# Kernel tuning notes

Hardware: AMD Instinct MI355X
Metric: run time of the kernel (lower is better)

## Reference

```python
import jax, jax.numpy as jnp
from jax import lax
import numpy as np

WIN = 9  # default window [9, 9] in the original module


def _box_sum(x, win):
    """Sum over a win x win window, stride 1, pad win//2 (same as conv2d with ones kernel).
    Implemented separably (two 1D convs) - mathematically identical to the 2D ones-kernel conv.
    x: [B, 1, H, W] float32.
    """
    pad = win // 2
    kh = jnp.ones((1, 1, win, 1), x.dtype)
    kw = jnp.ones((1, 1, 1, win), x.dtype)
    dn = lax.conv_dimension_numbers(x.shape, kh.shape, ('NCHW', 'OIHW', 'NCHW'))
    y = lax.conv_general_dilated(x, kh, (1, 1), [(pad, pad), (0, 0)], dimension_numbers=dn)
    return lax.conv_general_dilated(y, kw, (1, 1), [(0, 0), (pad, pad)], dimension_numbers=dn)


def setup_inputs() -> dict:
    key = jax.random.key(0)
    k1, k2 = jax.random.split(key)
    shape = (32, 1, 512, 512)
    predict = jax.random.uniform(k1, shape, dtype=jnp.float32)
    target = jax.random.uniform(k2, shape, dtype=jnp.float32)
    return {"predict": predict, "target": target}


def reference(predict, target):
    win = WIN
    win_size = jnp.asarray(win * win, jnp.float32)

    I, J = predict, target
    I_sum = _box_sum(I, win)
    J_sum = _box_sum(J, win)
    I2_sum = _box_sum(I * I, win)
    J2_sum = _box_sum(J * J, win)
    IJ_sum = _box_sum(I * J, win)

    u_I = I_sum / win_size
    u_J = J_sum / win_size

    cross = IJ_sum - u_J * I_sum - u_I * J_sum + u_I * u_J * win_size
    I_var = I2_sum - 2.0 * u_I * I_sum + u_I * u_I * win_size
    J_var = J2_sum - 2.0 * u_J * J_sum + u_J * u_J * win_size

    cc = cross * cross / (I_var * J_var + 1e-6)
    return -jnp.mean(cc) + 1.0
```

## Files before the change

### kernel.cpp

```cpp
#include <hip/hip_runtime.h>


#define W 512
#define H 512
#define BH 8
#define NBANDS (H / BH)
#define NT 64

__device__ __forceinline__ float4 ld4(const float* p) {
    return *reinterpret_cast<const float4*>(p);
}

#define DECLBUF(P) float4 P##A0, P##A1, P##B0, P##B1; float P##m

#define LOADR(P, DR) do {                                                    \
    int _r  = y0 + (DR);                                                     \
    int _rc = _r < 0 ? 0 : (_r > (H - 1) ? (H - 1) : _r);                    \
    const float* _ip = Ip + _rc * W + x0;                                    \
    const float* _jp = Jp + _rc * W + x0;                                    \
    P##A0 = ld4(_ip);  P##A1 = ld4(_ip + 4);                                 \
    P##B0 = ld4(_jp);  P##B1 = ld4(_jp + 4);                                 \
    P##m  = (_r == _rc) ? 1.f : 0.f;                                         \
} while (0)

#define PBODY(P, OP)                                                         \
    do {                                                                     \
        float _m = P##m;                                                     \
        float _a0=P##A0.x*_m, _a1=P##A0.y*_m, _a2=P##A0.z*_m, _a3=P##A0.w*_m;\
        float _a4=P##A1.x*_m, _a5=P##A1.y*_m, _a6=P##A1.z*_m, _a7=P##A1.w*_m;\
        float _b0=P##B0.x*_m, _b1=P##B0.y*_m, _b2=P##B0.z*_m, _b3=P##B0.w*_m;\
        float _b4=P##B1.x*_m, _b5=P##B1.y*_m, _b6=P##B1.z*_m, _b7=P##B1.w*_m;\
        v0[0] OP _a0; v0[1] OP _a1; v0[2] OP _a2; v0[3] OP _a3;              \
        v0[4] OP _a4; v0[5] OP _a5; v0[6] OP _a6; v0[7] OP _a7;              \
        v1[0] OP _b0; v1[1] OP _b1; v1[2] OP _b2; v1[3] OP _b3;              \
        v1[4] OP _b4; v1[5] OP _b5; v1[6] OP _b6; v1[7] OP _b7;              \
        v2[0] OP _a0*P##A0.x; v2[1] OP _a1*P##A0.y; v2[2] OP _a2*P##A0.z; v2[3] OP _a3*P##A0.w; \
        v2[4] OP _a4*P##A1.x; v2[5] OP _a5*P##A1.y; v2[6] OP _a6*P##A1.z; v2[7] OP _a7*P##A1.w; \
        v3[0] OP _b0*P##B0.x; v3[1] OP _b1*P##B0.y; v3[2] OP _b2*P##B0.z; v3[3] OP _b3*P##B0.w; \
        v3[4] OP _b4*P##B1.x; v3[5] OP _b5*P##B1.y; v3[6] OP _b6*P##B1.z; v3[7] OP _b7*P##B1.w; \
        v4[0] OP _a0*P##B0.x; v4[1] OP _a1*P##B0.y; v4[2] OP _a2*P##B0.z; v4[3] OP _a3*P##B0.w; \
        v4[4] OP _a4*P##B1.x; v4[5] OP _a5*P##B1.y; v4[6] OP _a6*P##B1.z; v4[7] OP _a7*P##B1.w; \
    } while (0)

#define PADD(P) PBODY(P, +=)
#define PSUB(P) PBODY(P, -=)

#define HLO(vv, h, l7out) do {                                               \
    float _l4 = __shfl_up(vv[4], 1), _l5 = __shfl_up(vv[5], 1);              \
    float _l6 = __shfl_up(vv[6], 1), _l7 = __shfl_up(vv[7], 1);              \
    if (lane == 0) { _l4 = 0.f; _l5 = 0.f; _l6 = 0.f; _l7 = 0.f; }           \
    float _t = (((_l4+_l5)+(_l6+_l7)) + ((vv[0]+vv[1])+(vv[2]+vv[3]))) + vv[4]; \
    h[0] = _t;                                                               \
    _t += vv[5] - _l4; h[1] = _t;                                            \
    _t += vv[6] - _l5; h[2] = _t;                                            \
    _t += vv[7] - _l6; h[3] = _t;                                            \
    l7out = _l7;                                                             \
} while (0)

#define HHI(vv, h3in, l7in, h) do {                                          \
    float _r0 = __shfl_down(vv[0], 1), _r1 = __shfl_down(vv[1], 1);          \
    float _r2 = __shfl_down(vv[2], 1), _r3 = __shfl_down(vv[3], 1);          \
    if (lane == 63) { _r0 = 0.f; _r1 = 0.f; _r2 = 0.f; _r3 = 0.f; }          \
    float _t = (h3in) + _r0 - (l7in); h[0] = _t;                             \
    _t += _r1 - vv[0]; h[1] = _t;                                            \
    _t += _r2 - vv[1]; h[2] = _t;                                            \
    _t += _r3 - vv[2]; h[3] = _t;                                            \
} while (0)

#define CC4(h0a, h1a, h2a, h3a, h4a) do {                                    \
    _Pragma("unroll")                                                        \
    for (int _c = 0; _c < 4; ++_c) {                                         \
        float _Is = h0a[_c], _Js = h1a[_c];                                  \
        float _u  = _Is * inv81;                                             \
        float _cr = h4a[_c] - _u * _Js;                                      \
        float _Iv = h2a[_c] - _u * _Is;                                      \
        float _Jv = h3a[_c] - (_Js * inv81) * _Js;                           \
        cc_acc += (_cr * _cr) * __builtin_amdgcn_rcpf(_Iv * _Jv + 1e-6f);    \
    }                                                                        \
} while (0)

#define EPI() do {                                                           \
    float h0[4], h1[4], h2[4], h3[4], h4[4];                                 \
    float s0, s1, s2, s3, s4;                                                \
    HLO(v0, h0, s0); HLO(v1, h1, s1); HLO(v2, h2, s2);                       \
    HLO(v3, h3, s3); HLO(v4, h4, s4);                                        \
    CC4(h0, h1, h2, h3, h4);                                                 \
    float e0 = h0[3], e1 = h1[3], e2 = h2[3], e3 = h3[3], e4 = h4[3];        \
    HHI(v0, e0, s0, h0); HHI(v1, e1, s1, h1); HHI(v2, e2, s2, h2);           \
    HHI(v3, e3, s3, h3); HHI(v4, e4, s4, h4);                                \
    CC4(h0, h1, h2, h3, h4);                                                 \
} while (0)

#define STEPL(AB, SB, DR) do { PADD(AB); EPI(); PSUB(SB); LOADR(SB, DR); } while (0)
#define STEPN(AB, SB)     do { PADD(AB); EPI(); PSUB(SB); } while (0)

__global__ __launch_bounds__(NT, 2)
void ncc_main(const float* __restrict__ I, const float* __restrict__ J,
              float* __restrict__ partials) {
    const int lane = threadIdx.x & 63;

    const int nblk = gridDim.x;
    const int g = (blockIdx.x & 7) * (nblk >> 3) + (blockIdx.x >> 3);

    const int b    = g >> 6;
    const int band = g & (NBANDS - 1);
    const int y0   = band * BH;
    const float* Ip = I + (size_t)b * (H * W);
    const float* Jp = J + (size_t)b * (H * W);
    const int x0 = lane * 8;

    float v0[8], v1[8], v2[8], v3[8], v4[8];
    #pragma unroll
    for (int k = 0; k < 8; ++k) { v0[k]=0.f; v1[k]=0.f; v2[k]=0.f; v3[k]=0.f; v4[k]=0.f; }

    float cc_acc = 0.f;
    const float inv81 = 1.f / 81.f;

    DECLBUF(B0); DECLBUF(B1); DECLBUF(B2); DECLBUF(B3); DECLBUF(B4);
    DECLBUF(B5); DECLBUF(B6); DECLBUF(B7); DECLBUF(B8); DECLBUF(B9);

    LOADR(B0, -4); LOADR(B1, -3); LOADR(B2, -2); LOADR(B3, -1);
    LOADR(B4,  0); LOADR(B5,  1); LOADR(B6,  2); LOADR(B7,  3);
    LOADR(B8,  4); LOADR(B9,  5);

    PADD(B0); PADD(B1); PADD(B2); PADD(B3);
    PADD(B4); PADD(B5); PADD(B6); PADD(B7);

    STEPL(B8, B0,  6);
    STEPL(B9, B1,  7);
    STEPL(B0, B2,  8);
    STEPL(B1, B3,  9);
    STEPL(B2, B4, 10);
    STEPL(B3, B5, 11);
    STEPN(B4, B6);
    STEPN(B5, B7);

    #pragma unroll
    for (int off = 32; off > 0; off >>= 1)
        cc_acc += __shfl_down(cc_acc, off, 64);
    if (lane == 0) partials[blockIdx.x] = cc_acc;
}

__global__ __launch_bounds__(256)
void ncc_finish(const float* __restrict__ partials, float* __restrict__ out,
                int n, float inv_total) {
    float v = 0.f;
    for (int i = threadIdx.x; i < n; i += blockDim.x) v += partials[i];
    #pragma unroll
    for (int off = 32; off > 0; off >>= 1)
        v += __shfl_down(v, off, 64);
    __shared__ float wsum[4];
    if ((threadIdx.x & 63) == 0) wsum[threadIdx.x >> 6] = v;
    __syncthreads();
    if (threadIdx.x == 0) {
        float t = (wsum[0] + wsum[1]) + (wsum[2] + wsum[3]);
        out[0] = 1.0f - t * inv_total;
    }
}

extern "C" void kernel_launch(void* const* d_in, const int* in_sizes, int n_in,
                              void* d_out, int out_size, void* d_ws, size_t ws_size,
                              hipStream_t stream) {
    const float* I = (const float*)d_in[0];
    const float* J = (const float*)d_in[1];
    float* out = (float*)d_out;
    float* partials = (float*)d_ws;

    const int n = in_sizes[0];
    const int B = n / (H * W);
    const int nblocks = B * NBANDS;

    ncc_main<<<nblocks, NT, 0, stream>>>(I, J, partials);
    ncc_finish<<<1, 256, 0, stream>>>(partials, out, nblocks, 1.0f / (float)n);
}
```

Measured before the change: 108.1 us.

## Widen row bands to 32 rows with deeper 12-row register prefetch ring

Each single-wavefront block now processes a 32-row band instead of 8, cutting halo re-reads from 8 extra rows per 8 output rows to 8 per 32. The sliding-window ring grows from 10 to 12 row buffers so loads are issued four steps ahead, and the min-blocks launch bound is dropped. Grid size falls fourfold, to 512 one-wave blocks, which lowers occupancy and parallelism on a GPU with many CUs. Register pressure also rises.

```diff
diff --git a/kernel.cpp b/kernel.cpp
--- a/kernel.cpp
+++ b/kernel.cpp
@@ -3,7 +3,7 @@
 
 #define W 512
 #define H 512
-#define BH 8
+#define BH 32
 #define NBANDS (H / BH)
 #define NT 64
 
@@ -94,7 +94,7 @@
 #define STEPL(AB, SB, DR) do { PADD(AB); EPI(); PSUB(SB); LOADR(SB, DR); } while (0)
 #define STEPN(AB, SB)     do { PADD(AB); EPI(); PSUB(SB); } while (0)
 
-__global__ __launch_bounds__(NT, 2)
+__global__ __launch_bounds__(NT)
 void ncc_main(const float* __restrict__ I, const float* __restrict__ J,
               float* __restrict__ partials) {
     const int lane = threadIdx.x & 63;
@@ -102,7 +102,7 @@
     const int nblk = gridDim.x;
     const int g = (blockIdx.x & 7) * (nblk >> 3) + (blockIdx.x >> 3);
 
-    const int b    = g >> 6;
+    const int b    = g >> 4;
     const int band = g & (NBANDS - 1);
     const int y0   = band * BH;
     const float* Ip = I + (size_t)b * (H * W);
@@ -116,24 +116,49 @@
     float cc_acc = 0.f;
     const float inv81 = 1.f / 81.f;
 
-    DECLBUF(B0); DECLBUF(B1); DECLBUF(B2); DECLBUF(B3); DECLBUF(B4);
-    DECLBUF(B5); DECLBUF(B6); DECLBUF(B7); DECLBUF(B8); DECLBUF(B9);
-
-    LOADR(B0, -4); LOADR(B1, -3); LOADR(B2, -2); LOADR(B3, -1);
-    LOADR(B4,  0); LOADR(B5,  1); LOADR(B6,  2); LOADR(B7,  3);
-    LOADR(B8,  4); LOADR(B9,  5);
+    DECLBUF(B0); DECLBUF(B1); DECLBUF(B2);  DECLBUF(B3);
+    DECLBUF(B4); DECLBUF(B5); DECLBUF(B6);  DECLBUF(B7);
+    DECLBUF(B8); DECLBUF(B9); DECLBUF(B10); DECLBUF(B11);
+
+    LOADR(B0, -4); LOADR(B1, -3); LOADR(B2,   -2); LOADR(B3,  -1);
+    LOADR(B4,  0); LOADR(B5,  1); LOADR(B6,    2); LOADR(B7,   3);
+    LOADR(B8,  4); LOADR(B9,  5); LOADR(B10,   6); LOADR(B11,  7);
 
     PADD(B0); PADD(B1); PADD(B2); PADD(B3);
     PADD(B4); PADD(B5); PADD(B6); PADD(B7);
 
-    STEPL(B8, B0,  6);
-    STEPL(B9, B1,  7);
-    STEPL(B0, B2,  8);
-    STEPL(B1, B3,  9);
-    STEPL(B2, B4, 10);
-    STEPL(B3, B5, 11);
-    STEPN(B4, B6);
-    STEPN(B5, B7);
+    STEPL(B8,  B0,   8);
+    STEPL(B9,  B1,   9);
+    STEPL(B10, B2,  10);
+    STEPL(B11, B3,  11);
+    STEPL(B0,  B4,  12);
+    STEPL(B1,  B5,  13);
+    STEPL(B2,  B6,  14);
+    STEPL(B3,  B7,  15);
+    STEPL(B4,  B8,  16);
+    STEPL(B5,  B9,  17);
+    STEPL(B6,  B10, 18);
+    STEPL(B7,  B11, 19);
+    STEPL(B8,  B0,  20);
+    STEPL(B9,  B1,  21);
+    STEPL(B10, B2,  22);
+    STEPL(B11, B3,  23);
+    STEPL(B0,  B4,  24);
+    STEPL(B1,  B5,  25);
+    STEPL(B2,  B6,  26);
+    STEPL(B3,  B7,  27);
+    STEPL(B4,  B8,  28);
+    STEPL(B5,  B9,  29);
+    STEPL(B6,  B10, 30);
+    STEPL(B7,  B11, 31);
+    STEPL(B8,  B0,  32);
+    STEPL(B9,  B1,  33);
+    STEPL(B10, B2,  34);
+    STEPL(B11, B3,  35);
+    STEPN(B0,  B4);
+    STEPN(B1,  B5);
+    STEPN(B2,  B6);
+    STEPN(B3,  B7);
 
     #pragma unroll
     for (int off = 32; off > 0; off >>= 1)
```

After: 122.0 us. 1.13x slower.

## Double band height and stream rows through small register ring with reloads

Applied to the files above, without the earlier changes.

The band height per wavefront goes from 8 to 16 rows, which halves the number of blocks and cuts the halo overhead (18 rows loaded per 8 output rows becomes 32 per 16). The 10-row register ring buffer is replaced by 6 buffers. Each step reloads both the incoming row and the outgoing row (for subtraction) instead of keeping all window rows in registers. This lowers register pressure but issues extra global loads for the subtracted rows, which should mostly hit cache, and it leaves fewer blocks to fill the GPU.

```diff
diff --git a/kernel.cpp b/kernel.cpp
--- a/kernel.cpp
+++ b/kernel.cpp
@@ -3,7 +3,7 @@
 
 #define W 512
 #define H 512
-#define BH 8
+#define BH 16
 #define NBANDS (H / BH)
 #define NT 64
 
@@ -91,8 +91,12 @@
     CC4(h0, h1, h2, h3, h4);                                                 \
 } while (0)
 
-#define STEPL(AB, SB, DR) do { PADD(AB); EPI(); PSUB(SB); LOADR(SB, DR); } while (0)
-#define STEPN(AB, SB)     do { PADD(AB); EPI(); PSUB(SB); } while (0)
+#define PR(P, DR) do { LOADR(P, DR); PADD(P); } while (0)
+
+#define STEP(PN, PO, I) do {                                                 \
+    LOADR(PN, (I) + 4); LOADR(PO, (I) - 4);                                  \
+    PADD(PN); EPI(); PSUB(PO);                                               \
+} while (0)
 
 __global__ __launch_bounds__(NT, 2)
 void ncc_main(const float* __restrict__ I, const float* __restrict__ J,
@@ -102,7 +106,7 @@
     const int nblk = gridDim.x;
     const int g = (blockIdx.x & 7) * (nblk >> 3) + (blockIdx.x >> 3);
 
-    const int b    = g >> 6;
+    const int b    = g >> 5;
     const int band = g & (NBANDS - 1);
     const int y0   = band * BH;
     const float* Ip = I + (size_t)b * (H * W);
@@ -116,24 +120,28 @@
     float cc_acc = 0.f;
     const float inv81 = 1.f / 81.f;
 
-    DECLBUF(B0); DECLBUF(B1); DECLBUF(B2); DECLBUF(B3); DECLBUF(B4);
-    DECLBUF(B5); DECLBUF(B6); DECLBUF(B7); DECLBUF(B8); DECLBUF(B9);
+    DECLBUF(P0); DECLBUF(P1); DECLBUF(P2);
+    DECLBUF(P3); DECLBUF(P4); DECLBUF(P5);
 
-    LOADR(B0, -4); LOADR(B1, -3); LOADR(B2, -2); LOADR(B3, -1);
-    LOADR(B4,  0); LOADR(B5,  1); LOADR(B6,  2); LOADR(B7,  3);
-    LOADR(B8,  4); LOADR(B9,  5);
+    PR(P0, -4); PR(P1, -3); PR(P2, -2); PR(P3, -1);
+    PR(P4,  0); PR(P5,  1); PR(P0,  2); PR(P1,  3);
 
-    PADD(B0); PADD(B1); PADD(B2); PADD(B3);
-    PADD(B4); PADD(B5); PADD(B6); PADD(B7);
-
-    STEPL(B8, B0,  6);
-    STEPL(B9, B1,  7);
-    STEPL(B0, B2,  8);
-    STEPL(B1, B3,  9);
-    STEPL(B2, B4, 10);
-    STEPL(B3, B5, 11);
-    STEPN(B4, B6);
-    STEPN(B5, B7);
+    STEP(P2, P3,  0);
+    STEP(P4, P5,  1);
+    STEP(P0, P1,  2);
+    STEP(P2, P3,  3);
+    STEP(P4, P5,  4);
+    STEP(P0, P1,  5);
+    STEP(P2, P3,  6);
+    STEP(P4, P5,  7);
+    STEP(P0, P1,  8);
+    STEP(P2, P3,  9);
+    STEP(P4, P5, 10);
+    STEP(P0, P1, 11);
+    STEP(P2, P3, 12);
+    STEP(P4, P5, 13);
+    STEP(P0, P1, 14);
+    STEP(P2, P3, 15);
 
     #pragma unroll
     for (int off = 32; off > 0; off >>= 1)
```

Result: slower. 115.3 us (+6.7%).
